# Performance work log

Hardware: AMD Instinct MI355X
Metric: run time of the kernel (lower is better)

## Reference

```python
import jax, jax.numpy as jnp
import numpy as np


def _clenshaw_curtiss(nlat):
    # equiangular nodes including poles: theta_k = pi*k/(n-1)
    n = nlat
    theta = np.pi * np.arange(n) / (n - 1)
    jmax = (n - 1) // 2
    j = np.arange(1, jmax + 1)
    b = np.where(2 * j == (n - 1), 1.0, 2.0)
    # v_k = 1 - sum_j b_j/(4j^2-1) cos(2 j theta_k)
    v = 1.0 - (b / (4.0 * j**2 - 1.0)) @ np.cos(2.0 * np.outer(j, theta))
    w = (2.0 / (n - 1)) * v
    w[0] *= 0.5
    w[-1] *= 0.5
    return theta, w  # quadrature on [-1,1], sum(w)=2


def _precompute_legpoly(mmax, lmax, theta, csphase=True):
    # orthonormal associated Legendre P_l^m(cos theta), shape (mmax, lmax, nlat)
    nlat = theta.shape[0]
    x = np.cos(theta)
    s = np.sin(theta)
    pct = np.zeros((mmax, lmax, nlat), dtype=np.float64)
    pmm = np.full(nlat, np.sqrt(1.0 / (4.0 * np.pi)))  # P_0^0
    sign = -1.0 if csphase else 1.0
    for m in range(mmax):
        if m > 0:
            pmm = sign * np.sqrt((2.0 * m + 1.0) / (2.0 * m)) * s * pmm
        if m < lmax:
            pct[m, m] = pmm
        if m + 1 < lmax:
            p_prev = pmm
            p = np.sqrt(2.0 * m + 3.0) * x * pmm
            pct[m, m + 1] = p
            for l in range(m + 2, lmax):
                a = np.sqrt((4.0 * l * l - 1.0) / (l * l - m * m))
                b = np.sqrt(((l - 1.0) ** 2 - m * m) / (4.0 * (l - 1.0) ** 2 - 1.0))
                p_new = a * (x * p - b * p_prev)
                pct[m, l] = p_new
                p_prev, p = p, p_new
    return pct


def _make_weights(nlat, lmax, mmax):
    theta, w = _clenshaw_curtiss(nlat)
    pct = _precompute_legpoly(mmax, lmax, theta, csphase=True)
    # fold quadrature weights in: 'mlk,k->mlk'
    return (pct * w[None, None, :]).astype(np.float32)


NLAT, NLON, LMAX, MMAX = 361, 720, 361, 361


def setup_inputs() -> dict:
    key = jax.random.key(0)
    x = jax.random.normal(key, (1, 256, NLAT, NLON), dtype=jnp.float32)
    weights = jnp.asarray(_make_weights(NLAT, LMAX, MMAX))  # (mmax, lmax, nlat)
    return {"x": x, "weights": weights}


def reference(x, weights):
    nlon = x.shape[-1]
    mmax = weights.shape[0]
    # rfft along longitude, 'forward' norm (divide by nlon), truncate to mmax, scale 2*pi
    xf = (2.0 * jnp.pi / nlon) * jnp.fft.rfft(x, axis=-1)[..., :mmax]  # (B,C,nlat,mmax)
    xr = jnp.swapaxes(xf.real, -1, -2)  # (B,C,mmax,nlat)
    xi = jnp.swapaxes(xf.imag, -1, -2)
    out_re = jnp.einsum('bcmk,mlk->bclm', xr, weights)  # (B,C,lmax,mmax)
    out_im = jnp.einsum('bcmk,mlk->bclm', xi, weights)
    return jax.lax.complex(out_re, out_im)
```

## Files before the change

### kernel.cpp

```cpp
#include <hip/hip_runtime.h>
#include <math.h>

#define TWO_PI 6.283185307179586f


typedef __attribute__((ext_vector_type(8))) short bf16x8;
typedef __attribute__((ext_vector_type(4))) float f32x4;

__device__ inline unsigned short f2bf(float f) {
    union { float f; unsigned int u; } v; v.f = f;
    unsigned int u = v.u;
    return (unsigned short)((u + 0x7fffu + ((u >> 16) & 1u)) >> 16);
}
__device__ inline float bf2f(unsigned short h) {
    union { unsigned int u; float f; } v; v.u = ((unsigned int)h) << 16;
    return v.f;
}
__device__ inline unsigned int packhl(float v) {
    unsigned short h = f2bf(v);
    unsigned short l = f2bf(v - bf2f(h));
    return (unsigned int)h | ((unsigned int)l << 16);
}
__device__ inline float unpackhl(unsigned int p) {
    return bf2f((unsigned short)(p & 0xffffu)) + bf2f((unsigned short)(p >> 16));
}
__device__ inline void split2(float a, float b, unsigned int& hh, unsigned int& ll) {
    unsigned short ha = f2bf(a), hb = f2bf(b);
    unsigned short la = f2bf(a - bf2f(ha)), lb = f2bf(b - bf2f(hb));
    hh = (unsigned int)ha | ((unsigned int)hb << 16);
    ll = (unsigned int)la | ((unsigned int)lb << 16);
}
__device__ inline void split2t(float a, float b, unsigned int& hh, unsigned int& ll) {
    union { float f; unsigned int u; } ua, ub, fa, fb, la, lb;
    ua.f = a; ub.f = b;
    hh = (ua.u >> 16) | (ub.u & 0xffff0000u);
    fa.u = ua.u & 0xffff0000u;
    fb.u = ub.u & 0xffff0000u;
    la.f = a - fa.f;
    lb.f = b - fb.f;
    ll = (la.u >> 16) | (lb.u & 0xffff0000u);
}
__device__ inline void gload_lds16(const void* g, void* l) {
    __builtin_amdgcn_global_load_lds(
        (const __attribute__((address_space(1))) unsigned int*)g,
        (__attribute__((address_space(3))) unsigned int*)l, 16, 0, 0);
}
__device__ inline int xcd_work(int bid, int nwg) {
    int q = nwg >> 3, r = nwg & 7;
    int xcd = bid & 7, ord = bid >> 3;
    return (xcd < r ? xcd * (q + 1) : r * (q + 1) + (xcd - r) * q) + ord;
}

__global__ void build_ect(unsigned short* __restrict__ Eh,
                          unsigned short* __restrict__ El) {
    const float sigma = TWO_PI / 720.0f;
    const int total = 384 * 192;
    for (int i = blockIdx.x * blockDim.x + threadIdx.x; i < total;
         i += gridDim.x * blockDim.x) {
        int row = i / 192, n = i % 192;
        int g = row / 192 ? 1 : 0;
        int mg = row - g * 192;
        int m = 2 * mg + g;
        float v = 0.f;
        if (m <= 360 && n <= 180) {
            int r = (n * m) % 720;
            v = sigma * cosf((float)r * (TWO_PI / 720.0f));
            if (n == 180) v *= 0.5f;
        }
        unsigned short h = f2bf(v);
        Eh[i] = h;
        El[i] = f2bf(v - bf2f(h));
    }
}

__global__ __launch_bounds__(256, 4) void s1_mfma(
    const float* __restrict__ x, const unsigned short* __restrict__ Eh,
    const unsigned short* __restrict__ El, unsigned int* __restrict__ xrp,
    const int Q) {
    __shared__ short Ah[2][4][64][8], Al[2][4][64][8];
    __shared__ short Bt[2][2][4][96][8];

    const int work = xcd_work(blockIdx.x, gridDim.x);
    const int q0 = (work >> 2) * 64;
    const int tt = work & 3;
    const int grp = tt >> 1;
    const int m0g = (tt & 1) * 96;
    const int t = threadIdx.x;
    const int lane = t & 63, wv = t >> 6;
    const int lr = lane & 15, lk = lane >> 4;
    const int wq = wv;

    const int ar = t >> 2, akc = t & 3;
    const int aq = q0 + ar;
    const float* arow = x + (size_t)aq * 720;
    const bool aqv = (aq < Q);

    const unsigned short* bsrc[3];
#pragma unroll
    for (int i = 0; i < 3; ++i) {
        int id = t + i * 256;
        int tab = id / 384, rem = id % 384;
        int kc = rem / 96, r = rem % 96;
        bsrc[i] = (tab ? El : Eh) + (size_t)(grp * 192 + m0g + r) * 192 + kc * 8;
    }

    f32x4 acc[6];
#pragma unroll
    for (int nj = 0; nj < 6; ++nj)
#pragma unroll
        for (int r = 0; r < 4; ++r) acc[nj][r] = 0.f;

    float4 f1a, f1b, f2a, f2b, r1a, r1b, r2a, r2b;

#define S1_LOADA(K0)                                                       \
    {                                                                      \
        int kg = (K0) + akc * 8;                                           \
        f1a = make_float4(0.f, 0.f, 0.f, 0.f);                             \
        f1b = f1a; f2a = f1a; f2b = f1a;                                   \
        r1a = f1a; r1b = f1a; r2a = f1a; r2b = f1a;                        \
        if (aqv) {                                                         \
            f1a = *(const float4*)(arow + kg);                             \
            f1b = *(const float4*)(arow + kg + 4);                         \
            f2a = *(const float4*)(arow + 360 + kg);                       \
            f2b = *(const float4*)(arow + 364 + kg);                       \
            r2a = *(const float4*)(arow + 353 - kg);                       \
            r2b = *(const float4*)(arow + 357 - kg);                       \
            if (kg >= 8) {                                                 \
                r1a = *(const float4*)(arow + 713 - kg);                   \
                r1b = *(const float4*)(arow + 717 - kg);                   \
            } else {                                                       \
                float tm[8];                                               \
                _Pragma("unroll") for (int i = 0; i < 8; ++i)              \
                    tm[i] = (7 - i >= 1) ? arow[713 + i] : 0.f;            \
                r1a = make_float4(tm[0], tm[1], tm[2], tm[3]);             \
                r1b = make_float4(tm[4], tm[5], tm[6], tm[7]);             \
            }                                                              \
        }                                                                  \
    }
#define S1_WRITEA(NB, K0)                                                  \
    {                                                                      \
        int kg = (K0) + akc * 8;                                           \
        float b0 = f1a.x + r1b.w, b1 = f1a.y + r1b.z;                      \
        float b2 = f1a.z + r1b.y, b3 = f1a.w + r1b.x;                      \
        float b4 = f1b.x + r1a.w, b5 = f1b.y + r1a.z;                      \
        float b6 = f1b.z + r1a.y, b7 = f1b.w + r1a.x;                      \
        float p0 = r2b.w + ((kg == 0) ? 0.f : f2a.x);                      \
        float p1 = r2b.z + f2a.y, p2 = r2b.y + f2a.z, p3 = r2b.x + f2a.w;  \
        float p4 = r2a.w + f2b.x, p5 = r2a.z + f2b.y;                      \
        float p6 = r2a.y + f2b.z, p7 = r2a.x + f2b.w;                      \
        float s = grp ? -1.f : 1.f;                                        \
        float y0 = b0 + s * p0, y1 = b1 + s * p1;                          \
        float y2 = b2 + s * p2, y3 = b3 + s * p3;                          \
        float y4 = b4 + s * p4, y5 = b5 + s * p5;                          \
        float y6 = b6 + s * p6, y7 = b7 + s * p7;                          \
        if (kg > 172) {                                                    \
            if (kg + 0 > 180) y0 = 0.f;                                    \
            if (kg + 1 > 180) y1 = 0.f;                                    \
            if (kg + 2 > 180) y2 = 0.f;                                    \
            if (kg + 3 > 180) y3 = 0.f;                                    \
            if (kg + 4 > 180) y4 = 0.f;                                    \
            if (kg + 5 > 180) y5 = 0.f;                                    \
            if (kg + 6 > 180) y6 = 0.f;                                    \
            if (kg + 7 > 180) y7 = 0.f;                                    \
        }                                                                  \
        unsigned int h0, h1, h2, h3, l0, l1, l2, l3;                      \
        split2t(y0, y1, h0, l0);                                          \
        split2t(y2, y3, h1, l1);                                          \
        split2t(y4, y5, h2, l2);                                          \
        split2t(y6, y7, h3, l3);                                          \
        *(uint4*)&Ah[NB][akc][ar][0] = make_uint4(h0, h1, h2, h3);        \
        *(uint4*)&Al[NB][akc][ar][0] = make_uint4(l0, l1, l2, l3);        \
    }
#define S1_COPYB(NB, K0)                                                  \
    {                                                                     \
        char* bb = (char*)&Bt[NB][0][0][0][0];                            \
        _Pragma("unroll") for (int i = 0; i < 3; ++i) {                   \
            gload_lds16(bsrc[i] + (K0), bb + (t + i * 256) * 16);         \
        }                                                                 \
    }

    S1_COPYB(0, 0);
    S1_LOADA(0);
    S1_WRITEA(0, 0);
    __syncthreads();
    int cur = 0;
    const int NIT = 6;
    for (int it = 0; it < NIT; ++it) {
        const int nb = cur ^ 1;
        if (it + 1 < NIT) {
            S1_COPYB(nb, (it + 1) * 32);
            S1_LOADA((it + 1) * 32);
        }
        bf16x8 ah = *(const bf16x8*)&Ah[cur][lk][wq * 16 + lr][0];
        bf16x8 al = *(const bf16x8*)&Al[cur][lk][wq * 16 + lr][0];
#pragma unroll
        for (int nj = 0; nj < 6; ++nj) {
            bf16x8 bh = *(const bf16x8*)&Bt[cur][0][lk][nj * 16 + lr][0];
            bf16x8 bl = *(const bf16x8*)&Bt[cur][1][lk][nj * 16 + lr][0];
            acc[nj] = __builtin_amdgcn_mfma_f32_16x16x32_bf16(ah, bh, acc[nj], 0, 0, 0);
            acc[nj] = __builtin_amdgcn_mfma_f32_16x16x32_bf16(ah, bl, acc[nj], 0, 0, 0);
            acc[nj] = __builtin_amdgcn_mfma_f32_16x16x32_bf16(al, bh, acc[nj], 0, 0, 0);
        }
        if (it + 1 < NIT) {
            S1_WRITEA(nb, (it + 1) * 32);
            __syncthreads();
            cur = nb;
        }
    }

#pragma unroll
    for (int nj = 0; nj < 6; ++nj) {
        int mg = m0g + nj * 16 + lr;
        int m = 2 * mg + grp;
        if (m >= 361) continue;
        size_t base = (size_t)m * Q;
#pragma unroll
        for (int reg = 0; reg < 4; ++reg) {
            int q = q0 + wq * 16 + lk * 4 + reg;
            if (q < Q) xrp[base + q] = packhl(acc[nj][reg]);
        }
    }
}

__global__ __launch_bounds__(256) void fold_uv(const unsigned int* __restrict__ xrp,
                                               unsigned int* __restrict__ up,
                                               unsigned int* __restrict__ vp,
                                               const int CH) {
    const int total = 361 * CH * 192;
    const int Q = CH * 361;
    for (int i = blockIdx.x * blockDim.x + threadIdx.x; i < total;
         i += gridDim.x * blockDim.x) {
        int m = i / (CH * 192);
        int rem = i - m * (CH * 192);
        int bc = rem / 192;
        int k = rem - bc * 192;
        float u = 0.f, v = 0.f;
        if (k <= 180) {
            size_t base = (size_t)m * Q + (size_t)bc * 361;
            float x1 = unpackhl(xrp[base + k]);
            if (k < 180) {
                float x2 = unpackhl(xrp[base + 360 - k]);
                u = x1 + x2;
                v = x1 - x2;
            } else {
                u = x1;
                v = x1;
            }
        }
        up[i] = packhl(u);
        vp[i] = packhl(v);
    }
}

__global__ __launch_bounds__(256, 4) void s2_mfma(
    const unsigned int* __restrict__ up, const unsigned int* __restrict__ vp,
    const float* __restrict__ W, float* __restrict__ stg, const int CH) {
    __shared__ short Ah[128][40], Al[128][40];
    __shared__ short Bh[64][40], Bl[64][40];

    const int work = xcd_work(blockIdx.x, gridDim.x);
    const int m = work / 12;
    const int rem = work % 12;
    const int half = rem / 6;
    const int r2 = rem % 6;
    const int g = r2 / 3, lgt = r2 % 3;
    const int lg0 = lgt * 64;
    const int par = (g + m) & 1;
    if (2 * (lg0 + 63) + par < m) return;
    const int bcbase = half * 128;
    if (bcbase >= CH) return;
    const int t = threadIdx.x;
    const int lane = t & 63, wv = t >> 6;
    const int lr = lane & 15, lk = lane >> 4;
    const int wbc = wv >> 1, wl = wv & 1;

    const unsigned int* Am = (g ? vp : up) + (size_t)m * CH * 192;
    const float* Wm = W + (size_t)m * 130321;

    f32x4 acc[4][2];
#pragma unroll
    for (int fi = 0; fi < 4; ++fi)
#pragma unroll
        for (int ni = 0; ni < 2; ++ni)
#pragma unroll
            for (int r = 0; r < 4; ++r) acc[fi][ni][r] = 0.f;

    unsigned int pa0[8], pa1[8];
    float wva[4], wvb[4];

#define S2_LOADR(K0)                                                          \
    {                                                                         \
        _Pragma("unroll") for (int i = 0; i < 8; ++i) {                       \
            int id = t + i * 256;                                             \
            int r = id >> 4, kp = id & 15;                                    \
            int bc = bcbase + r, kg = (K0) + kp * 2;                          \
            unsigned int p0 = 0, p1 = 0;                                      \
            if (bc < CH) {                                                    \
                size_t base = (size_t)bc * 192;                               \
                p0 = Am[base + kg];                                           \
                p1 = Am[base + kg + 1];                                       \
            }                                                                 \
            pa0[i] = p0; pa1[i] = p1;                                         \
        }                                                                     \
        _Pragma("unroll") for (int i = 0; i < 4; ++i) {                       \
            int id = t + i * 256;                                             \
            int r = id >> 4, kp = id & 15;                                    \
            int l = 2 * (lg0 + r) + par, kg = (K0) + kp * 2;                  \
            float va = 0.f, vb = 0.f;                                         \
            if (l < 361) {                                                    \
                size_t base = (size_t)l * 361;                                \
                if (kg <= 180) va = Wm[base + kg];                            \
                if (kg + 1 <= 180) vb = Wm[base + kg + 1];                    \
            }                                                                 \
            wva[i] = va; wvb[i] = vb;                                         \
        }                                                                     \
    }
#define S2_WRITES()                                                           \
    {                                                                         \
        _Pragma("unroll") for (int i = 0; i < 8; ++i) {                       \
            int id = t + i * 256;                                             \
            int r = id >> 4, kp = id & 15;                                    \
            *(unsigned int*)&Ah[r][kp * 2] =                                  \
                (pa0[i] & 0xffffu) | (pa1[i] << 16);                          \
            *(unsigned int*)&Al[r][kp * 2] =                                  \
                (pa0[i] >> 16) | (pa1[i] & 0xffff0000u);                      \
        }                                                                     \
        _Pragma("unroll") for (int i = 0; i < 4; ++i) {                       \
            int id = t + i * 256;                                             \
            int r = id >> 4, kp = id & 15;                                    \
            unsigned int hh, ll;                                              \
            split2(wva[i], wvb[i], hh, ll);                                   \
            *(unsigned int*)&Bh[r][kp * 2] = hh;                              \
            *(unsigned int*)&Bl[r][kp * 2] = ll;                              \
        }                                                                     \
    }

    S2_LOADR(0);
    S2_WRITES();
    __syncthreads();
    for (int it = 0; it < 6; ++it) {
        if (it + 1 < 6) S2_LOADR((it + 1) * 32);
#pragma unroll
        for (int fi = 0; fi < 4; ++fi) {
            bf16x8 ah = *(const bf16x8*)&Ah[wbc * 64 + fi * 16 + lr][lk * 8];
            bf16x8 al = *(const bf16x8*)&Al[wbc * 64 + fi * 16 + lr][lk * 8];
#pragma unroll
            for (int ni = 0; ni < 2; ++ni) {
                bf16x8 bh = *(const bf16x8*)&Bh[wl * 32 + ni * 16 + lr][lk * 8];
                bf16x8 bl = *(const bf16x8*)&Bl[wl * 32 + ni * 16 + lr][lk * 8];
                acc[fi][ni] = __builtin_amdgcn_mfma_f32_16x16x32_bf16(ah, bh, acc[fi][ni], 0, 0, 0);
                acc[fi][ni] = __builtin_amdgcn_mfma_f32_16x16x32_bf16(ah, bl, acc[fi][ni], 0, 0, 0);
                acc[fi][ni] = __builtin_amdgcn_mfma_f32_16x16x32_bf16(al, bh, acc[fi][ni], 0, 0, 0);
            }
        }
        __syncthreads();
        if (it + 1 < 6) {
            S2_WRITES();
            __syncthreads();
        }
    }

#pragma unroll
    for (int fi = 0; fi < 4; ++fi) {
#pragma unroll
        for (int ni = 0; ni < 2; ++ni) {
            int l = 2 * (lg0 + wl * 32 + ni * 16 + lr) + par;
#pragma unroll
            for (int reg = 0; reg < 4; ++reg) {
                int bc = bcbase + wbc * 64 + fi * 16 + lk * 4 + reg;
                if (bc < CH && l < 361)
                    stg[((size_t)m * CH + bc) * 361 + l] = acc[fi][ni][reg];
            }
        }
    }
}

__global__ __launch_bounds__(256) void transpose_out(const float* __restrict__ stg,
                                                     float* __restrict__ out,
                                                     const int c0, const int CH) {
    __shared__ float tile[32][33];
    const int Q = CH * 361;
    const int m0 = blockIdx.y * 32, q0 = blockIdx.x * 32;
    const int tx = threadIdx.x & 31, ty = threadIdx.x >> 5;
    for (int i = ty; i < 32; i += 8) {
        int mm = m0 + i, q = q0 + tx;
        float v = 0.f;
        if (mm < 361 && q < Q) {
            int l = q % 361;
            int par = l & 1;
            int lg = l >> 1;
            if (2 * (lg | 63) + par >= mm) v = stg[(size_t)mm * Q + q];
        }
        tile[i][tx] = v;
    }
    __syncthreads();
    for (int i = ty; i < 32; i += 8) {
        int q = q0 + i, mm = m0 + tx;
        if (mm < 361 && q < Q)
            out[((size_t)c0 * 361 + q) * 361 + mm] = tile[tx][i];
    }
}

extern "C" void kernel_launch(void* const* d_in, const int* in_sizes, int n_in,
                              void* d_out, int out_size, void* d_ws, size_t ws_size,
                              hipStream_t stream) {
    (void)out_size;
    const float* x = (const float*)d_in[0];
    const float* W = (const float*)d_in[1];
    if (n_in >= 2 && (in_sizes[0] == 47045881 || in_sizes[1] == 66539520)) {
        x = (const float*)d_in[1];
        W = (const float*)d_in[0];
    }
    float* out = (float*)d_out;

    const size_t offEh = 0;
    const size_t offEl = 147456;
    const size_t offData = 294912;

    const int cands[6] = {256, 128, 64, 32, 16, 8};
    int CH = 0;
    for (int i = 0; i < 6; ++i) {
        size_t need = offData + (size_t)cands[i] * (130321ull * 2 + 69312ull * 2) * 4;
        if (need <= ws_size) { CH = cands[i]; break; }
    }
    if (!CH) return;

    unsigned short* Eh = (unsigned short*)((char*)d_ws + offEh);
    unsigned short* El = (unsigned short*)((char*)d_ws + offEl);
    unsigned int* xrp = (unsigned int*)((char*)d_ws + offData);
    unsigned int* up = xrp + (size_t)CH * 130321;
    unsigned int* vp = up + (size_t)CH * 69312;
    float* stg = (float*)(vp + (size_t)CH * 69312);

    build_ect<<<256, 256, 0, stream>>>(Eh, El);

    const int Q = CH * 361;
    const int qt = (Q + 63) / 64;
    for (int c0 = 0; c0 < 256; c0 += CH) {
        s1_mfma<<<qt * 4, 256, 0, stream>>>(
            x + (size_t)c0 * 361 * 720, Eh, El, xrp, Q);
        fold_uv<<<8192, 256, 0, stream>>>(xrp, up, vp, CH);
        s2_mfma<<<361 * 12, 256, 0, stream>>>(up, vp, W, stg, CH);
        transpose_out<<<dim3((Q + 31) / 32, 12), 256, 0, stream>>>(stg, out, c0, CH);
    }
}
```

Baseline: 542.8 us.

## Preload full DFT tile to LDS and build A fragments in registers

The stage-1 DFT GEMM now loads its entire 64-row bf16 hi/lo cosine table slice into padded shared memory once. Each lane then forms its A-operand fragment (folded symmetric input samples split into hi/lo bf16) directly in registers, which removes the per-iteration A staging through LDS, the double buffering and the barriers in the k-loop. The output tile shrinks from 96 to 64 m-columns, so the grid grows from 4 to 6 tiles per q-block and occupancy is lowered to 3 blocks. The trade-off is that each block re-reads and re-folds the input rows, and the more numerous tiles repeat that work more often.

```diff
diff --git a/kernel.cpp b/kernel.cpp
--- a/kernel.cpp
+++ b/kernel.cpp
@@ -6,6 +6,8 @@
 
 typedef __attribute__((ext_vector_type(8))) short bf16x8;
 typedef __attribute__((ext_vector_type(4))) float f32x4;
+
+union BFU { uint4 u; bf16x8 v; };
 
 __device__ inline unsigned short f2bf(float f) {
     union { float f; unsigned int u; } v; v.f = f;
@@ -73,150 +75,107 @@
     }
 }
 
-__global__ __launch_bounds__(256, 4) void s1_mfma(
+__global__ __launch_bounds__(256, 3) void s1_mfma(
     const float* __restrict__ x, const unsigned short* __restrict__ Eh,
     const unsigned short* __restrict__ El, unsigned int* __restrict__ xrp,
     const int Q) {
-    __shared__ short Ah[2][4][64][8], Al[2][4][64][8];
-    __shared__ short Bt[2][2][4][96][8];
+    __shared__ short Bt[2][64][200];
 
     const int work = xcd_work(blockIdx.x, gridDim.x);
-    const int q0 = (work >> 2) * 64;
-    const int tt = work & 3;
-    const int grp = tt >> 1;
-    const int m0g = (tt & 1) * 96;
+    const int q0 = (work / 6) * 64;
+    const int tile = work % 6;
+    const int grp = tile / 3;
+    const int m0t = (tile % 3) * 64;
     const int t = threadIdx.x;
     const int lane = t & 63, wv = t >> 6;
     const int lr = lane & 15, lk = lane >> 4;
-    const int wq = wv;
-
-    const int ar = t >> 2, akc = t & 3;
-    const int aq = q0 + ar;
-    const float* arow = x + (size_t)aq * 720;
-    const bool aqv = (aq < Q);
-
-    const unsigned short* bsrc[3];
-#pragma unroll
-    for (int i = 0; i < 3; ++i) {
+
+#pragma unroll
+    for (int i = 0; i < 13; ++i) {
         int id = t + i * 256;
-        int tab = id / 384, rem = id % 384;
-        int kc = rem / 96, r = rem % 96;
-        bsrc[i] = (tab ? El : Eh) + (size_t)(grp * 192 + m0g + r) * 192 + kc * 8;
-    }
-
-    f32x4 acc[6];
-#pragma unroll
-    for (int nj = 0; nj < 6; ++nj)
+        if (id < 3200) {
+            int tab = id / 1600, rem = id % 1600;
+            int row = rem / 25, c = rem % 25;
+            int cs = (c < 24) ? c : 23;
+            const unsigned short* src =
+                (tab ? El : Eh) + (size_t)(grp * 192 + m0t + row) * 192 + cs * 8;
+            gload_lds16(src, (char*)&Bt[0][0][0] + id * 16);
+        }
+    }
+    __syncthreads();
+
+    const int aq = q0 + wv * 16 + lr;
+    const bool qv = (aq < Q);
+    const float* arow = x + (size_t)(qv ? aq : 0) * 720;
+    const float sgn = grp ? -1.f : 1.f;
+
+    f32x4 acc[4];
+#pragma unroll
+    for (int nj = 0; nj < 4; ++nj)
 #pragma unroll
         for (int r = 0; r < 4; ++r) acc[nj][r] = 0.f;
 
-    float4 f1a, f1b, f2a, f2b, r1a, r1b, r2a, r2b;
-
-#define S1_LOADA(K0)                                                       \
-    {                                                                      \
-        int kg = (K0) + akc * 8;                                           \
-        f1a = make_float4(0.f, 0.f, 0.f, 0.f);                             \
-        f1b = f1a; f2a = f1a; f2b = f1a;                                   \
-        r1a = f1a; r1b = f1a; r2a = f1a; r2b = f1a;                        \
-        if (aqv) {                                                         \
-            f1a = *(const float4*)(arow + kg);                             \
-            f1b = *(const float4*)(arow + kg + 4);                         \
-            f2a = *(const float4*)(arow + 360 + kg);                       \
-            f2b = *(const float4*)(arow + 364 + kg);                       \
-            r2a = *(const float4*)(arow + 353 - kg);                       \
-            r2b = *(const float4*)(arow + 357 - kg);                       \
-            if (kg >= 8) {                                                 \
-                r1a = *(const float4*)(arow + 713 - kg);                   \
-                r1b = *(const float4*)(arow + 717 - kg);                   \
-            } else {                                                       \
-                float tm[8];                                               \
-                _Pragma("unroll") for (int i = 0; i < 8; ++i)              \
-                    tm[i] = (7 - i >= 1) ? arow[713 + i] : 0.f;            \
-                r1a = make_float4(tm[0], tm[1], tm[2], tm[3]);             \
-                r1b = make_float4(tm[4], tm[5], tm[6], tm[7]);             \
-            }                                                              \
-        }                                                                  \
-    }
-#define S1_WRITEA(NB, K0)                                                  \
-    {                                                                      \
-        int kg = (K0) + akc * 8;                                           \
-        float b0 = f1a.x + r1b.w, b1 = f1a.y + r1b.z;                      \
-        float b2 = f1a.z + r1b.y, b3 = f1a.w + r1b.x;                      \
-        float b4 = f1b.x + r1a.w, b5 = f1b.y + r1a.z;                      \
-        float b6 = f1b.z + r1a.y, b7 = f1b.w + r1a.x;                      \
-        float p0 = r2b.w + ((kg == 0) ? 0.f : f2a.x);                      \
-        float p1 = r2b.z + f2a.y, p2 = r2b.y + f2a.z, p3 = r2b.x + f2a.w;  \
-        float p4 = r2a.w + f2b.x, p5 = r2a.z + f2b.y;                      \
-        float p6 = r2a.y + f2b.z, p7 = r2a.x + f2b.w;                      \
-        float s = grp ? -1.f : 1.f;                                        \
-        float y0 = b0 + s * p0, y1 = b1 + s * p1;                          \
-        float y2 = b2 + s * p2, y3 = b3 + s * p3;                          \
-        float y4 = b4 + s * p4, y5 = b5 + s * p5;                          \
-        float y6 = b6 + s * p6, y7 = b7 + s * p7;                          \
-        if (kg > 172) {                                                    \
-            if (kg + 0 > 180) y0 = 0.f;                                    \
-            if (kg + 1 > 180) y1 = 0.f;                                    \
-            if (kg + 2 > 180) y2 = 0.f;                                    \
-            if (kg + 3 > 180) y3 = 0.f;                                    \
-            if (kg + 4 > 180) y4 = 0.f;                                    \
-            if (kg + 5 > 180) y5 = 0.f;                                    \
-            if (kg + 6 > 180) y6 = 0.f;                                    \
-            if (kg + 7 > 180) y7 = 0.f;                                    \
-        }                                                                  \
-        unsigned int h0, h1, h2, h3, l0, l1, l2, l3;                      \
-        split2t(y0, y1, h0, l0);                                          \
-        split2t(y2, y3, h1, l1);                                          \
-        split2t(y4, y5, h2, l2);                                          \
-        split2t(y6, y7, h3, l3);                                          \
-        *(uint4*)&Ah[NB][akc][ar][0] = make_uint4(h0, h1, h2, h3);        \
-        *(uint4*)&Al[NB][akc][ar][0] = make_uint4(l0, l1, l2, l3);        \
-    }
-#define S1_COPYB(NB, K0)                                                  \
-    {                                                                     \
-        char* bb = (char*)&Bt[NB][0][0][0][0];                            \
-        _Pragma("unroll") for (int i = 0; i < 3; ++i) {                   \
-            gload_lds16(bsrc[i] + (K0), bb + (t + i * 256) * 16);         \
-        }                                                                 \
-    }
-
-    S1_COPYB(0, 0);
-    S1_LOADA(0);
-    S1_WRITEA(0, 0);
-    __syncthreads();
-    int cur = 0;
-    const int NIT = 6;
-    for (int it = 0; it < NIT; ++it) {
-        const int nb = cur ^ 1;
-        if (it + 1 < NIT) {
-            S1_COPYB(nb, (it + 1) * 32);
-            S1_LOADA((it + 1) * 32);
-        }
-        bf16x8 ah = *(const bf16x8*)&Ah[cur][lk][wq * 16 + lr][0];
-        bf16x8 al = *(const bf16x8*)&Al[cur][lk][wq * 16 + lr][0];
-#pragma unroll
-        for (int nj = 0; nj < 6; ++nj) {
-            bf16x8 bh = *(const bf16x8*)&Bt[cur][0][lk][nj * 16 + lr][0];
-            bf16x8 bl = *(const bf16x8*)&Bt[cur][1][lk][nj * 16 + lr][0];
+#pragma unroll
+    for (int it = 0; it < 6; ++it) {
+        const int n0 = it * 32 + lk * 8;
+        float4 fa = *(const float4*)(arow + n0);
+        float4 fb = *(const float4*)(arow + n0 + 4);
+        float4 ga = *(const float4*)(arow + 360 + n0);
+        float4 gb = *(const float4*)(arow + 364 + n0);
+        float4 sa = *(const float4*)(arow + 353 - n0);
+        float4 sb = *(const float4*)(arow + 357 - n0);
+        float4 ra, rb;
+        if (n0 >= 8) {
+            ra = *(const float4*)(arow + 713 - n0);
+            rb = *(const float4*)(arow + 717 - n0);
+        } else {
+            float tm[8];
+#pragma unroll
+            for (int i = 0; i < 8; ++i)
+                tm[i] = (7 - i >= 1) ? arow[713 + i] : 0.f;
+            ra = make_float4(tm[0], tm[1], tm[2], tm[3]);
+            rb = make_float4(tm[4], tm[5], tm[6], tm[7]);
+        }
+        float f[8] = {fa.x, fa.y, fa.z, fa.w, fb.x, fb.y, fb.z, fb.w};
+        float g[8] = {ga.x, ga.y, ga.z, ga.w, gb.x, gb.y, gb.z, gb.w};
+        float rv[8] = {rb.w, rb.z, rb.y, rb.x, ra.w, ra.z, ra.y, ra.x};
+        float sv[8] = {sb.w, sb.z, sb.y, sb.x, sa.w, sa.z, sa.y, sa.x};
+        float y[8];
+#pragma unroll
+        for (int j = 0; j < 8; ++j) {
+            int n = n0 + j;
+            float base = f[j] + rv[j];
+            float pair = sv[j] + ((n == 0) ? 0.f : g[j]);
+            float val = base + sgn * pair;
+            y[j] = (qv && n <= 180) ? val : 0.f;
+        }
+        BFU hu, lu;
+        split2t(y[0], y[1], hu.u.x, lu.u.x);
+        split2t(y[2], y[3], hu.u.y, lu.u.y);
+        split2t(y[4], y[5], hu.u.z, lu.u.z);
+        split2t(y[6], y[7], hu.u.w, lu.u.w);
+        const bf16x8 ah = hu.v, al = lu.v;
+
+#pragma unroll
+        for (int nj = 0; nj < 4; ++nj) {
+            const int brow = nj * 16 + lr;
+            bf16x8 bh = *(const bf16x8*)&Bt[0][brow][it * 32 + lk * 8];
+            bf16x8 bl = *(const bf16x8*)&Bt[1][brow][it * 32 + lk * 8];
             acc[nj] = __builtin_amdgcn_mfma_f32_16x16x32_bf16(ah, bh, acc[nj], 0, 0, 0);
             acc[nj] = __builtin_amdgcn_mfma_f32_16x16x32_bf16(ah, bl, acc[nj], 0, 0, 0);
             acc[nj] = __builtin_amdgcn_mfma_f32_16x16x32_bf16(al, bh, acc[nj], 0, 0, 0);
         }
-        if (it + 1 < NIT) {
-            S1_WRITEA(nb, (it + 1) * 32);
-            __syncthreads();
-            cur = nb;
-        }
-    }
-
-#pragma unroll
-    for (int nj = 0; nj < 6; ++nj) {
-        int mg = m0g + nj * 16 + lr;
+    }
+
+#pragma unroll
+    for (int nj = 0; nj < 4; ++nj) {
+        int mg = m0t + nj * 16 + lr;
         int m = 2 * mg + grp;
         if (m >= 361) continue;
         size_t base = (size_t)m * Q;
 #pragma unroll
         for (int reg = 0; reg < 4; ++reg) {
-            int q = q0 + wq * 16 + lk * 4 + reg;
+            int q = q0 + wv * 16 + lk * 4 + reg;
             if (q < Q) xrp[base + q] = packhl(acc[nj][reg]);
         }
     }
@@ -437,7 +396,7 @@
     const int Q = CH * 361;
     const int qt = (Q + 63) / 64;
     for (int c0 = 0; c0 < 256; c0 += CH) {
-        s1_mfma<<<qt * 4, 256, 0, stream>>>(
+        s1_mfma<<<qt * 6, 256, 0, stream>>>(
             x + (size_t)c0 * 361 * 720, Eh, El, xrp, Q);
         fold_uv<<<8192, 256, 0, stream>>>(xrp, up, vp, CH);
         s2_mfma<<<361 * 12, 256, 0, stream>>>(up, vp, W, stg, CH);
```

Result: slower. 617.0 us (+13.7%).
